# Kernel optimization log

Hardware: AMD Instinct MI355X
Metric: run time of the kernel (lower is better)

## Reference

```python
import jax, jax.numpy as jnp
import numpy as np

B, L, K, I, O = 4, 10000, 16, 256, 256


def setup_inputs() -> dict:
    key = jax.random.key(0)
    k1, k2, k3 = jax.random.split(key, 3)
    x = jax.random.normal(k1, (B, L, I), dtype=jnp.float32)
    index_tensor = jax.random.randint(k2, (L, K), 0, L, dtype=jnp.int64)
    stdv = 0.5
    mask = jax.random.uniform(k3, (K, I, O), dtype=jnp.float32, minval=-stdv, maxval=stdv)
    bias = jnp.zeros((O,), dtype=jnp.float32)
    return {"x": x, "index_tensor": index_tensor, "mask": mask, "bias": bias}


def reference(x, index_tensor, mask, bias):
    # torch: expand x to [b,l,l,i], gather along dim2 with index[l,k] -> [b,l,k,i]
    # equivalent: per output node n, neighbors x[:, index_tensor[n, j], :]
    gathered = x[:, index_tensor, :]            # [b, l, k, i]
    # flatten(k,i) @ flatten(mask: [k*i, o]) == einsum over k,i
    y = jnp.einsum('blki,kio->blo', gathered, mask) + bias
    return y
```

## Files before the change

kernel.cpp:

```cpp
#include <hip/hip_runtime.h>

#define Bdim 4
#define Ldim 10000
#define Kdim 16
#define Idim 256
#define Odim 256

typedef __attribute__((ext_vector_type(8))) __bf16 bf16x8;
typedef __attribute__((ext_vector_type(4))) float f32x4;

__global__ __launch_bounds__(256)
void convert_x(const float* __restrict__ x, __bf16* __restrict__ xb)
{
    const size_t base = ((size_t)blockIdx.x * 256 + threadIdx.x) * 16;
#pragma unroll
    for (int j = 0; j < 2; ++j) {
        const float4 f0 = *(const float4*)(x + base + j * 8);
        const float4 f1 = *(const float4*)(x + base + j * 8 + 4);
        bf16x8 v;
        v[0] = (__bf16)f0.x; v[1] = (__bf16)f0.y; v[2] = (__bf16)f0.z; v[3] = (__bf16)f0.w;
        v[4] = (__bf16)f1.x; v[5] = (__bf16)f1.y; v[6] = (__bf16)f1.z; v[7] = (__bf16)f1.w;
        *(bf16x8*)(xb + base + j * 8) = v;
    }
}

__global__ __launch_bounds__(256)
void convert_mask(const float* __restrict__ mask, __bf16* __restrict__ wt)
{
    __shared__ float lds[32][33];
    const int t  = threadIdx.x;
    const int r  = t >> 5;
    const int c  = t & 31;
    const int kk0 = blockIdx.x * 32;
    const int o0  = blockIdx.y * 32;
#pragma unroll
    for (int rr = r; rr < 32; rr += 8)
        lds[rr][c] = mask[(size_t)(kk0 + rr) * Odim + o0 + c];
    __syncthreads();
#pragma unroll
    for (int rr = r; rr < 32; rr += 8)
        wt[(size_t)(o0 + rr) * (Kdim * Idim) + kk0 + c] = (__bf16)lds[c][rr];
}

#define TL 16
#define BM 64
#define BN 256
#define LDA 72

__global__ __launch_bounds__(256, 3)
void piconv_gemm(const __bf16* __restrict__ xb,
                 const int* __restrict__ idxT,
                 const __bf16* __restrict__ wt,
                 const float* __restrict__ bias,
                 float* __restrict__ out)
{
    __shared__ __bf16 Alds[BM * LDA];
    __shared__ __bf16 Wlds[BN * LDA];
    __shared__ int    idx_lds[TL][Kdim];

    const int t  = threadIdx.x;
    const int l0 = blockIdx.x * TL;

    const int lane = t & 63;
    const int wid  = t >> 6;
    const int q    = lane >> 4;
    const int r16  = lane & 15;

    {
        const int lt = t >> 4, k = t & 15;
        idx_lds[lt][k] = idxT[(l0 + lt) * Kdim + k];
    }

    const int arow  = t >> 2;
    const int apart = t & 3;
    const int alt   = arow & 15;
    const int abb   = arow >> 4;
    const size_t abase = ((size_t)abb * Ldim) << 8;

    const __bf16* wp = wt + (((size_t)(t >> 3)) << 12) + (t & 7) * 8;

    f32x4 acc[4][4] = {};
    bf16x8 aN[2], wN[8];

    __syncthreads();

    {
        const int iv = idx_lds[alt][0];
        const __bf16* src = xb + abase + (((size_t)iv) << 8) + apart * 16;
        aN[0] = *(const bf16x8*)src;
        aN[1] = *(const bf16x8*)(src + 8);
#pragma unroll
        for (int it = 0; it < 8; ++it)
            wN[it] = *(const bf16x8*)(wp + ((size_t)it << 17));
    }

    for (int kb = 0; kb < 64; ++kb) {
        *(bf16x8*)&Alds[arow * LDA + apart * 16]     = aN[0];
        *(bf16x8*)&Alds[arow * LDA + apart * 16 + 8] = aN[1];
#pragma unroll
        for (int it = 0; it < 8; ++it)
            *(bf16x8*)&Wlds[(it * 32 + (t >> 3)) * LDA + (t & 7) * 8] = wN[it];
        __syncthreads();

        if (kb < 63) {
            const int kn = (kb + 1) >> 2;
            const int io = (((kb + 1) & 3) << 6) + apart * 16;
            const int iv = idx_lds[alt][kn];
            const __bf16* src = xb + abase + (((size_t)iv) << 8) + io;
            aN[0] = *(const bf16x8*)src;
            aN[1] = *(const bf16x8*)(src + 8);
            const __bf16* wq = wp + (kb + 1) * 64;
#pragma unroll
            for (int it = 0; it < 8; ++it)
                wN[it] = *(const bf16x8*)(wq + ((size_t)it << 17));
        }

#pragma unroll
        for (int ks = 0; ks < 2; ++ks) {
            bf16x8 af[4], bfr[4];
#pragma unroll
            for (int mi = 0; mi < 4; ++mi)
                af[mi] = *(bf16x8*)&Alds[(mi * 16 + r16) * LDA + ks * 32 + q * 8];
#pragma unroll
            for (int ni = 0; ni < 4; ++ni)
                bfr[ni] = *(bf16x8*)&Wlds[(wid * 64 + ni * 16 + r16) * LDA + ks * 32 + q * 8];
#pragma unroll
            for (int mi = 0; mi < 4; ++mi)
#pragma unroll
                for (int ni = 0; ni < 4; ++ni)
                    acc[mi][ni] = __builtin_amdgcn_mfma_f32_16x16x32_bf16(
                        af[mi], bfr[ni], acc[mi][ni], 0, 0, 0);
        }
        __syncthreads();
    }

    float bv[4];
#pragma unroll
    for (int ni = 0; ni < 4; ++ni)
        bv[ni] = bias[wid * 64 + ni * 16 + r16];
#pragma unroll
    for (int mi = 0; mi < 4; ++mi) {
#pragma unroll
        for (int rr = 0; rr < 4; ++rr) {
            const int lt = q * 4 + rr;
            float* dst = out + (((size_t)(mi * Ldim + l0 + lt)) << 8) + wid * 64 + r16;
#pragma unroll
            for (int ni = 0; ni < 4; ++ni)
                dst[ni * 16] = acc[mi][ni][rr] + bv[ni];
        }
    }
}

#define FTL 32
#define FBN 128
#define FLDA 72
__global__ __launch_bounds__(256)
void piconv_fallback(const float* __restrict__ x,
                     const int* __restrict__ idxT,
                     const float* __restrict__ mask,
                     const float* __restrict__ bias,
                     float* __restrict__ out)
{
    __shared__ __bf16 Alds[128 * FLDA];
    __shared__ __bf16 Wlds[FBN * FLDA];
    const int t  = threadIdx.x;
    const int l0 = blockIdx.x * FTL;
    const int n0 = blockIdx.y * FBN;
    const int lane = t & 63;
    const int wid  = t >> 6;
    const int wm   = wid >> 1;
    const int wn   = wid & 1;
    const int q    = lane >> 4;
    const int r16  = lane & 15;
    f32x4 acc[4][4] = {};
    const int am    = t >> 1;
    const int ahalf = t & 1;
    const int alt   = am & 31;
    const int abb   = am >> 5;
    const int al    = l0 + alt;
    const bool avalid = (al < Ldim);
    for (int kb = 0; kb < 64; ++kb) {
        {
            const int ksl = kb >> 2;
            const int i0  = ((kb & 3) << 6) + (ahalf << 5);
            const int idx = avalid ? idxT[al * Kdim + ksl] : 0;
            const float* src = x + (((size_t)(abb * Ldim + idx)) << 8) + i0;
#pragma unroll
            for (int j = 0; j < 4; ++j) {
                const float4 f0 = *(const float4*)(src + j * 8);
                const float4 f1 = *(const float4*)(src + j * 8 + 4);
                bf16x8 v;
                v[0] = (__bf16)f0.x; v[1] = (__bf16)f0.y; v[2] = (__bf16)f0.z; v[3] = (__bf16)f0.w;
                v[4] = (__bf16)f1.x; v[5] = (__bf16)f1.y; v[6] = (__bf16)f1.z; v[7] = (__bf16)f1.w;
                *(bf16x8*)&Alds[am * FLDA + (ahalf << 5) + j * 8] = v;
            }
        }
        {
#pragma unroll
            for (int it = 0; it < 4; ++it) {
                const int pair = t + it * 256;
                const int n    = pair & 127;
                const int g    = pair >> 7;
                const float* src = mask + (((size_t)(kb * 64 + g * 8)) << 8) + n0 + n;
                bf16x8 v;
#pragma unroll
                for (int j = 0; j < 8; ++j)
                    v[j] = (__bf16)src[(size_t)j << 8];
                *(bf16x8*)&Wlds[n * FLDA + g * 8] = v;
            }
        }
        __syncthreads();
#pragma unroll
        for (int ks = 0; ks < 2; ++ks) {
            bf16x8 af[4], bfr[4];
#pragma unroll
            for (int mi = 0; mi < 4; ++mi)
                af[mi] = *(bf16x8*)&Alds[(wm * 64 + mi * 16 + r16) * FLDA + ks * 32 + q * 8];
#pragma unroll
            for (int ni = 0; ni < 4; ++ni)
                bfr[ni] = *(bf16x8*)&Wlds[(wn * 64 + ni * 16 + r16) * FLDA + ks * 32 + q * 8];
#pragma unroll
            for (int mi = 0; mi < 4; ++mi)
#pragma unroll
                for (int ni = 0; ni < 4; ++ni)
                    acc[mi][ni] = __builtin_amdgcn_mfma_f32_16x16x32_bf16(
                        af[mi], bfr[ni], acc[mi][ni], 0, 0, 0);
        }
        __syncthreads();
    }
    float bv[4];
#pragma unroll
    for (int ni = 0; ni < 4; ++ni)
        bv[ni] = bias[n0 + wn * 64 + ni * 16 + r16];
#pragma unroll
    for (int mi = 0; mi < 4; ++mi) {
        const int mrow = wm * 64 + mi * 16 + q * 4;
#pragma unroll
        for (int rr = 0; rr < 4; ++rr) {
            const int m  = mrow + rr;
            const int lt = m & 31;
            const int bb = m >> 5;
            const int l  = l0 + lt;
            if (l < Ldim) {
                float* dst = out + (((size_t)(bb * Ldim + l)) << 8) + n0 + wn * 64 + r16;
#pragma unroll
                for (int ni = 0; ni < 4; ++ni)
                    dst[ni * 16] = acc[mi][ni][rr] + bv[ni];
            }
        }
    }
}

extern "C" void kernel_launch(void* const* d_in, const int* in_sizes, int n_in,
                              void* d_out, int out_size, void* d_ws, size_t ws_size,
                              hipStream_t stream) {
    const float* x    = (const float*)d_in[0];
    const int*   idx  = (const int*)d_in[1];
    const float* mask = (const float*)d_in[2];
    const float* bias = (const float*)d_in[3];
    float* out = (float*)d_out;

    const size_t xb_bytes = (size_t)Bdim * Ldim * Idim * 2;
    const size_t wt_bytes = (size_t)Kdim * Idim * Odim * 2;

    if (ws_size >= xb_bytes + wt_bytes) {
        __bf16* xb = (__bf16*)d_ws;
        __bf16* wt = (__bf16*)((char*)d_ws + xb_bytes);
        convert_x<<<(Bdim * Ldim * Idim) / (256 * 16), 256, 0, stream>>>(x, xb);
        convert_mask<<<dim3((Kdim * Idim) / 32, Odim / 32), 256, 0, stream>>>(mask, wt);
        piconv_gemm<<<Ldim / TL, 256, 0, stream>>>(xb, idx, wt, bias, out);
    } else {
        dim3 grid((Ldim + FTL - 1) / FTL, Odim / FBN, 1);
        piconv_fallback<<<grid, 256, 0, stream>>>(x, idx, mask, bias, out);
    }
}
```

Measured before the change: 219.1 us.

## Prepack weights in MFMA fragment order and load B operands directly to registers

Merges the x and mask conversion kernels into one prepack launch that writes the mask in per-wave MFMA fragment order. The GEMM kernel then reads weight fragments straight from global memory into registers, double-buffered across steps, instead of staging a 256x72 weight tile in LDS. The A tile moves to a double-buffered LDS layout, which removes one barrier per k-step. This cuts LDS traffic and synchronisation and frees LDS for occupancy, at the cost of more registers and uncoalesced strided mask reads in the prepack.

```diff
diff --git a/kernel.cpp b/kernel.cpp
--- a/kernel.cpp
+++ b/kernel.cpp
@@ -10,66 +10,61 @@
 typedef __attribute__((ext_vector_type(4))) float f32x4;
 
 __global__ __launch_bounds__(256)
-void convert_x(const float* __restrict__ x, __bf16* __restrict__ xb)
+void prepack(const float* __restrict__ x, const float* __restrict__ mask,
+             __bf16* __restrict__ xb, __bf16* __restrict__ wpk)
 {
-    const size_t base = ((size_t)blockIdx.x * 256 + threadIdx.x) * 16;
-#pragma unroll
-    for (int j = 0; j < 2; ++j) {
-        const float4 f0 = *(const float4*)(x + base + j * 8);
-        const float4 f1 = *(const float4*)(x + base + j * 8 + 4);
+    const int b = blockIdx.x;
+    if (b < 2500) {
+        const size_t base = ((size_t)b * 256 + threadIdx.x) * 16;
+#pragma unroll
+        for (int j = 0; j < 2; ++j) {
+            const float4 f0 = *(const float4*)(x + base + j * 8);
+            const float4 f1 = *(const float4*)(x + base + j * 8 + 4);
+            bf16x8 v;
+            v[0] = (__bf16)f0.x; v[1] = (__bf16)f0.y; v[2] = (__bf16)f0.z; v[3] = (__bf16)f0.w;
+            v[4] = (__bf16)f1.x; v[5] = (__bf16)f1.y; v[6] = (__bf16)f1.z; v[7] = (__bf16)f1.w;
+            *(bf16x8*)(xb + base + j * 8) = v;
+        }
+    } else {
+        const int tg = (b - 2500) * 256 + threadIdx.x;
+        const int c  = tg >> 6;
+        const int ln = tg & 63;
+        const int ni  = c & 3;
+        const int ks  = (c >> 2) & 1;
+        const int wid = (c >> 3) & 3;
+        const int kb  = c >> 5;
+        const int n   = wid * 64 + ni * 16 + (ln & 15);
+        const int kk0 = kb * 64 + ks * 32 + (ln >> 4) * 8;
         bf16x8 v;
-        v[0] = (__bf16)f0.x; v[1] = (__bf16)f0.y; v[2] = (__bf16)f0.z; v[3] = (__bf16)f0.w;
-        v[4] = (__bf16)f1.x; v[5] = (__bf16)f1.y; v[6] = (__bf16)f1.z; v[7] = (__bf16)f1.w;
-        *(bf16x8*)(xb + base + j * 8) = v;
-    }
-}
-
-__global__ __launch_bounds__(256)
-void convert_mask(const float* __restrict__ mask, __bf16* __restrict__ wt)
-{
-    __shared__ float lds[32][33];
-    const int t  = threadIdx.x;
-    const int r  = t >> 5;
-    const int c  = t & 31;
-    const int kk0 = blockIdx.x * 32;
-    const int o0  = blockIdx.y * 32;
-#pragma unroll
-    for (int rr = r; rr < 32; rr += 8)
-        lds[rr][c] = mask[(size_t)(kk0 + rr) * Odim + o0 + c];
-    __syncthreads();
-#pragma unroll
-    for (int rr = r; rr < 32; rr += 8)
-        wt[(size_t)(o0 + rr) * (Kdim * Idim) + kk0 + c] = (__bf16)lds[c][rr];
+#pragma unroll
+        for (int j = 0; j < 8; ++j)
+            v[j] = (__bf16)mask[(size_t)(kk0 + j) * Odim + n];
+        *(bf16x8*)(wpk + (size_t)tg * 8) = v;
+    }
 }
 
 #define TL 16
 #define BM 64
-#define BN 256
 #define LDA 72
 
 __global__ __launch_bounds__(256, 3)
 void piconv_gemm(const __bf16* __restrict__ xb,
                  const int* __restrict__ idxT,
-                 const __bf16* __restrict__ wt,
+                 const __bf16* __restrict__ wpk,
                  const float* __restrict__ bias,
                  float* __restrict__ out)
 {
-    __shared__ __bf16 Alds[BM * LDA];
-    __shared__ __bf16 Wlds[BN * LDA];
-    __shared__ int    idx_lds[TL][Kdim];
-
-    const int t  = threadIdx.x;
-    const int l0 = blockIdx.x * TL;
-
+    __shared__ __bf16 Alds[2][BM * LDA];
+    __shared__ int    idx_lds[TL * Kdim];
+
+    const int t    = threadIdx.x;
+    const int l0   = blockIdx.x * TL;
     const int lane = t & 63;
     const int wid  = t >> 6;
     const int q    = lane >> 4;
     const int r16  = lane & 15;
 
-    {
-        const int lt = t >> 4, k = t & 15;
-        idx_lds[lt][k] = idxT[(l0 + lt) * Kdim + k];
-    }
+    idx_lds[t] = idxT[l0 * Kdim + t];
 
     const int arow  = t >> 2;
     const int apart = t & 3;
@@ -77,62 +72,60 @@
     const int abb   = arow >> 4;
     const size_t abase = ((size_t)abb * Ldim) << 8;
 
-    const __bf16* wp = wt + (((size_t)(t >> 3)) << 12) + (t & 7) * 8;
-
-    f32x4 acc[4][4] = {};
-    bf16x8 aN[2], wN[8];
+    const __bf16* wbase = wpk + ((size_t)(wid * 8) << 9) + lane * 8;
+
+    f32x4  acc[4][4] = {};
+    bf16x8 aN0, aN1, wA[8], wB[8];
 
     __syncthreads();
 
     {
-        const int iv = idx_lds[alt][0];
-        const __bf16* src = xb + abase + (((size_t)iv) << 8) + apart * 16;
-        aN[0] = *(const bf16x8*)src;
-        aN[1] = *(const bf16x8*)(src + 8);
-#pragma unroll
-        for (int it = 0; it < 8; ++it)
-            wN[it] = *(const bf16x8*)(wp + ((size_t)it << 17));
-    }
-
-    for (int kb = 0; kb < 64; ++kb) {
-        *(bf16x8*)&Alds[arow * LDA + apart * 16]     = aN[0];
-        *(bf16x8*)&Alds[arow * LDA + apart * 16 + 8] = aN[1];
-#pragma unroll
-        for (int it = 0; it < 8; ++it)
-            *(bf16x8*)&Wlds[(it * 32 + (t >> 3)) * LDA + (t & 7) * 8] = wN[it];
-        __syncthreads();
-
-        if (kb < 63) {
-            const int kn = (kb + 1) >> 2;
-            const int io = (((kb + 1) & 3) << 6) + apart * 16;
-            const int iv = idx_lds[alt][kn];
-            const __bf16* src = xb + abase + (((size_t)iv) << 8) + io;
-            aN[0] = *(const bf16x8*)src;
-            aN[1] = *(const bf16x8*)(src + 8);
-            const __bf16* wq = wp + (kb + 1) * 64;
-#pragma unroll
-            for (int it = 0; it < 8; ++it)
-                wN[it] = *(const bf16x8*)(wq + ((size_t)it << 17));
-        }
-
-#pragma unroll
-        for (int ks = 0; ks < 2; ++ks) {
-            bf16x8 af[4], bfr[4];
-#pragma unroll
-            for (int mi = 0; mi < 4; ++mi)
-                af[mi] = *(bf16x8*)&Alds[(mi * 16 + r16) * LDA + ks * 32 + q * 8];
-#pragma unroll
-            for (int ni = 0; ni < 4; ++ni)
-                bfr[ni] = *(bf16x8*)&Wlds[(wid * 64 + ni * 16 + r16) * LDA + ks * 32 + q * 8];
-#pragma unroll
-            for (int mi = 0; mi < 4; ++mi)
-#pragma unroll
-                for (int ni = 0; ni < 4; ++ni)
-                    acc[mi][ni] = __builtin_amdgcn_mfma_f32_16x16x32_bf16(
-                        af[mi], bfr[ni], acc[mi][ni], 0, 0, 0);
-        }
-        __syncthreads();
-    }
+        const int iv = idx_lds[alt * Kdim];
+        const __bf16* s = xb + abase + (((size_t)iv) << 8) + apart * 16;
+        aN0 = *(const bf16x8*)s;
+        aN1 = *(const bf16x8*)(s + 8);
+#pragma unroll
+        for (int j = 0; j < 8; ++j)
+            wA[j] = *(const bf16x8*)(wbase + j * 512);
+    }
+
+#define STEP(KB, BUF, WCUR, WNXT, PF)                                           \
+    {                                                                           \
+        *(bf16x8*)&Alds[BUF][arow * LDA + apart * 16]     = aN0;                \
+        *(bf16x8*)&Alds[BUF][arow * LDA + apart * 16 + 8] = aN1;                \
+        __syncthreads();                                                        \
+        if (PF) {                                                               \
+            const int kn = ((KB) + 1) >> 2;                                     \
+            const int io = ((((KB) + 1) & 3) << 6) + apart * 16;                \
+            const int iv = idx_lds[alt * Kdim + kn];                            \
+            const __bf16* s = xb + abase + (((size_t)iv) << 8) + io;            \
+            aN0 = *(const bf16x8*)s;                                            \
+            aN1 = *(const bf16x8*)(s + 8);                                      \
+            const __bf16* wq = wbase + ((size_t)((KB) + 1)) * 16384;            \
+            _Pragma("unroll")                                                   \
+            for (int j = 0; j < 8; ++j)                                         \
+                WNXT[j] = *(const bf16x8*)(wq + j * 512);                       \
+        }                                                                       \
+        _Pragma("unroll")                                                       \
+        for (int ks = 0; ks < 2; ++ks) {                                        \
+            bf16x8 af[4];                                                       \
+            _Pragma("unroll")                                                   \
+            for (int mi = 0; mi < 4; ++mi)                                      \
+                af[mi] = *(bf16x8*)&Alds[BUF][(mi * 16 + r16) * LDA + ks * 32 + q * 8]; \
+            _Pragma("unroll")                                                   \
+            for (int mi = 0; mi < 4; ++mi)                                      \
+                _Pragma("unroll")                                               \
+                for (int ni = 0; ni < 4; ++ni)                                  \
+                    acc[mi][ni] = __builtin_amdgcn_mfma_f32_16x16x32_bf16(      \
+                        af[mi], WCUR[ks * 4 + ni], acc[mi][ni], 0, 0, 0);       \
+        }                                                                       \
+    }
+
+    for (int kb2 = 0; kb2 < 32; ++kb2) {
+        STEP(2 * kb2,     0, wA, wB, true)
+        STEP(2 * kb2 + 1, 1, wB, wA, (2 * kb2 + 1) < 63)
+    }
+#undef STEP
 
     float bv[4];
 #pragma unroll
@@ -261,14 +254,13 @@
     float* out = (float*)d_out;
 
     const size_t xb_bytes = (size_t)Bdim * Ldim * Idim * 2;
-    const size_t wt_bytes = (size_t)Kdim * Idim * Odim * 2;
-
-    if (ws_size >= xb_bytes + wt_bytes) {
-        __bf16* xb = (__bf16*)d_ws;
-        __bf16* wt = (__bf16*)((char*)d_ws + xb_bytes);
-        convert_x<<<(Bdim * Ldim * Idim) / (256 * 16), 256, 0, stream>>>(x, xb);
-        convert_mask<<<dim3((Kdim * Idim) / 32, Odim / 32), 256, 0, stream>>>(mask, wt);
-        piconv_gemm<<<Ldim / TL, 256, 0, stream>>>(xb, idx, wt, bias, out);
+    const size_t wp_bytes = (size_t)Kdim * Idim * Odim * 2;
+
+    if (ws_size >= xb_bytes + wp_bytes) {
+        __bf16* xb  = (__bf16*)d_ws;
+        __bf16* wpk = (__bf16*)((char*)d_ws + xb_bytes);
+        prepack<<<2500 + 512, 256, 0, stream>>>(x, mask, xb, wpk);
+        piconv_gemm<<<Ldim / TL, 256, 0, stream>>>(xb, idx, wpk, bias, out);
     } else {
         dim3 grid((Ldim + FTL - 1) / FTL, Odim / FBN, 1);
         piconv_fallback<<<grid, 256, 0, stream>>>(x, idx, mask, bias, out);
```

New measurement: 187.8 us. -14.3%, faster.
